# Kernel tuning notes

Hardware: AMD Instinct MI355X
Metric: run time of the kernel (lower is better)

Reference implementation:

```python
import jax, jax.numpy as jnp
import numpy as np

N = 100000
E = 1600000
F_IN, F_HID, F_OUT = 128, 64, 1


def setup_inputs() -> dict:
    key = jax.random.key(0)
    ks = jax.random.split(key, 8)
    x = jax.random.normal(ks[0], (N, F_IN), dtype=jnp.float32)
    edge_index = jax.random.randint(ks[1], (2, E), 0, N, dtype=jnp.int64)
    def glorot(k, fan_in, fan_out):
        scale = jnp.sqrt(2.0 / (fan_in + fan_out)).astype(jnp.float32)
        return jax.random.normal(k, (fan_in, fan_out), dtype=jnp.float32) * scale
    W1 = glorot(ks[2], F_IN, F_HID); b1 = jnp.zeros((F_HID,), jnp.float32)
    W2 = glorot(ks[3], F_HID, F_HID); b2 = jnp.zeros((F_HID,), jnp.float32)
    W3 = glorot(ks[4], F_HID, F_OUT); b3 = jnp.zeros((F_OUT,), jnp.float32)
    return {"x": x, "W1": W1, "b1": b1, "W2": W2, "b2": b2, "W3": W3, "b3": b3, "edge_index": edge_index}


def _gcn_norm(edge_index, n):
    # add self-loops, symmetric D^{-1/2} (A+I) D^{-1/2} normalization (PyG GCNConv default)
    loop = jnp.arange(n, dtype=edge_index.dtype)
    src = jnp.concatenate([edge_index[0], loop])
    dst = jnp.concatenate([edge_index[1], loop])
    deg = jax.ops.segment_sum(jnp.ones_like(src, dtype=jnp.float32), dst, num_segments=n)
    dis = jnp.where(deg > 0, jax.lax.rsqrt(jnp.maximum(deg, 1.0)), 0.0)
    norm = dis[src] * dis[dst]  # [E+N]
    return src, dst, norm


def _gcn_conv(h, W, b, src, dst, norm, n):
    h = h @ W                                   # [N, f_out]
    msg = h[src] * norm[:, None]                # gather + scale, [E+N, f_out]
    out = jax.ops.segment_sum(msg, dst, num_segments=n)  # scatter-add
    return out + b


def reference(x, W1, b1, W2, b2, W3, b3, edge_index):
    n = x.shape[0]
    src, dst, norm = _gcn_norm(edge_index, n)
    h = jax.nn.relu(_gcn_conv(x, W1, b1, src, dst, norm, n))
    h = jax.nn.relu(_gcn_conv(h, W2, b2, src, dst, norm, n))
    h = _gcn_conv(h, W3, b3, src, dst, norm, n)
    return jax.nn.sigmoid(h)
```

## Files before the change

kernel.cpp:

```cpp
#include <hip/hip_runtime.h>
#include <math.h>

#define NN 100000
#define NE 1600000
#define NSHARD 4
#define SHARD_W (NN / NSHARD)
#define NCHUNK 64
#define CHUNK_E (NE / NCHUNK)
#define CHUNK_I4 (CHUNK_E / 4)

typedef __attribute__((ext_vector_type(8))) short bf16x8;
typedef __attribute__((ext_vector_type(4))) float f32x4;
typedef __attribute__((ext_vector_type(2))) float f32x2;

__device__ inline unsigned f2bf(float f) {
    unsigned u = __float_as_uint(f);
    u += 0x7FFFu + ((u >> 16) & 1u);
    return u >> 16;
}
__device__ inline float bflo(unsigned v) { return __uint_as_float(v << 16); }
__device__ inline float bfhi(unsigned v) { return __uint_as_float(v & 0xFFFF0000u); }
__device__ inline f32x2 bfpair(unsigned u) {
    f32x2 r;
    r.x = __uint_as_float(u << 16);
    r.y = __uint_as_float(u & 0xFFFF0000u);
    return r;
}

__global__ __launch_bounds__(256) void k_cnt(const int4* __restrict__ dst4,
                                             unsigned char* __restrict__ cnt,
                                             unsigned char* __restrict__ lrank) {
    __shared__ __align__(16) unsigned ldeg[SHARD_W];
    int t = threadIdx.x;
    int shard = blockIdx.x & (NSHARD - 1);
    int b = blockIdx.x >> 2;
    int lo = shard * SHARD_W;
    uint4 z4 = make_uint4(0u, 0u, 0u, 0u);
    for (int i = t; i < SHARD_W / 4; i += 256) ((uint4*)ldeg)[i] = z4;
    __syncthreads();
    const int4* p = dst4 + b * CHUNK_I4;
    unsigned char* lr = lrank + b * CHUNK_E;
#pragma unroll 4
    for (int j = t; j < CHUNK_I4; j += 256) {
        int4 d = p[j];
        unsigned ex = (unsigned)(d.x - lo);
        unsigned ey = (unsigned)(d.y - lo);
        unsigned ez = (unsigned)(d.z - lo);
        unsigned ew = (unsigned)(d.w - lo);
        if (ex < SHARD_W) lr[4 * j + 0] = (unsigned char)atomicAdd(&ldeg[ex], 1u);
        if (ey < SHARD_W) lr[4 * j + 1] = (unsigned char)atomicAdd(&ldeg[ey], 1u);
        if (ez < SHARD_W) lr[4 * j + 2] = (unsigned char)atomicAdd(&ldeg[ez], 1u);
        if (ew < SHARD_W) lr[4 * j + 3] = (unsigned char)atomicAdd(&ldeg[ew], 1u);
    }
    __syncthreads();
    unsigned* cb32 = (unsigned*)cnt + b * (NN / 4) + shard * (SHARD_W / 4);
    for (int i = t; i < SHARD_W / 4; i += 256) {
        uint4 v = *(const uint4*)&ldeg[4 * i];
        cb32[i] = (v.x & 255u) | ((v.y & 255u) << 8) | ((v.z & 255u) << 16)
                | ((v.w & 255u) << 24);
    }
}

__global__ __launch_bounds__(256) void k_blkscan(unsigned char* __restrict__ cnt,
                                                 int* __restrict__ deg,
                                                 int* __restrict__ bsums) {
    __shared__ int s[256];
    int i = blockIdx.x * 256 + threadIdx.x;
    int total = 0;
    if (i < NN) {
        unsigned a = 0;
#pragma unroll
        for (int b = 0; b < NCHUNK; ++b) {
            unsigned v = cnt[b * NN + i];
            cnt[b * NN + i] = (unsigned char)a;
            a += v;
        }
        deg[i] = (int)a;
        total = (int)a;
    }
    s[threadIdx.x] = total;
    __syncthreads();
    for (int off = 128; off > 0; off >>= 1) {
        if (threadIdx.x < off) s[threadIdx.x] += s[threadIdx.x + off];
        __syncthreads();
    }
    if (threadIdx.x == 0) bsums[blockIdx.x] = s[0];
}

__global__ void k_scan512(const int* __restrict__ bsums, int* __restrict__ bscan) {
    __shared__ int s[512];
    int t = threadIdx.x;
    int v = (t < 391) ? bsums[t] : 0;
    s[t] = v;
    __syncthreads();
    for (int off = 1; off < 512; off <<= 1) {
        int x = (t >= off) ? s[t - off] : 0;
        __syncthreads();
        s[t] += x;
        __syncthreads();
    }
    bscan[t] = s[t] - v;
}

__global__ void k_rowptr(const int* __restrict__ deg, const int* __restrict__ bscan,
                         int* __restrict__ rowptr, float* __restrict__ dis) {
    __shared__ int s[256];
    int t = threadIdx.x;
    int i = blockIdx.x * 256 + t;
    int d = (i < NN) ? deg[i] : 0;
    s[t] = d;
    __syncthreads();
    for (int off = 1; off < 256; off <<= 1) {
        int x = (t >= off) ? s[t - off] : 0;
        __syncthreads();
        s[t] += x;
        __syncthreads();
    }
    if (i < NN) {
        int rp = bscan[blockIdx.x] + s[t] - d;
        rowptr[i] = rp;
        dis[i] = rsqrtf((float)(d + 1));
    }
    if (i == 0) rowptr[NN] = NE;
}

__global__ __launch_bounds__(256) void k_build_csr(
    const int4* __restrict__ src4, const int4* __restrict__ dst4,
    const unsigned char* __restrict__ blkoff, const unsigned* __restrict__ lr4,
    const int* __restrict__ rowptr, int* __restrict__ csr) {
    int shard = blockIdx.x & (NSHARD - 1);
    int bsh = blockIdx.x >> 2;
    int stride = (gridDim.x >> 2) * 256;
    int lo = shard * SHARD_W;
    const int NE4 = NE / 4;
    for (int i = bsh * 256 + threadIdx.x; i < NE4; i += stride) {
        int4 d = dst4[i];
        int4 s = src4[i];
        unsigned lr = lr4[i];
        const unsigned char* off = blkoff + (i / CHUNK_I4) * NN;
        unsigned ex = (unsigned)(d.x - lo);
        unsigned ey = (unsigned)(d.y - lo);
        unsigned ez = (unsigned)(d.z - lo);
        unsigned ew = (unsigned)(d.w - lo);
        if (ex < SHARD_W) csr[rowptr[d.x] + off[d.x] + (lr & 255u)] = s.x;
        if (ey < SHARD_W) csr[rowptr[d.y] + off[d.y] + ((lr >> 8) & 255u)] = s.y;
        if (ez < SHARD_W) csr[rowptr[d.z] + off[d.z] + ((lr >> 16) & 255u)] = s.z;
        if (ew < SHARD_W) csr[rowptr[d.w] + off[d.w] + (lr >> 24)] = s.w;
    }
}

#define XS_LD 136
__global__ __launch_bounds__(256) void k_gemm1(
    const float* __restrict__ x, const float* __restrict__ W,
    const float* __restrict__ dis, unsigned short* __restrict__ tsb) {
    __shared__ unsigned short xs[64 * XS_LD];
    __shared__ unsigned short wt[64 * XS_LD];
    int t = threadIdx.x;
    int row0 = blockIdx.x * 64;
    for (int i = t; i < 64 * 64; i += 256) {
        int n = i & 63, k2 = i >> 6;
        float w0 = W[(2 * k2) * 64 + n];
        float w1 = W[(2 * k2 + 1) * 64 + n];
        *(unsigned*)&wt[n * XS_LD + 2 * k2] = f2bf(w0) | (f2bf(w1) << 16);
    }
    for (int i = t; i < 64 * 32; i += 256) {
        int r = i >> 5, c4 = i & 31;
        int gr = row0 + r;
        uint2 p = {0u, 0u};
        if (gr < NN) {
            float4 v = *(const float4*)&x[gr * 128 + 4 * c4];
            p.x = f2bf(v.x) | (f2bf(v.y) << 16);
            p.y = f2bf(v.z) | (f2bf(v.w) << 16);
        }
        *(uint2*)&xs[r * XS_LD + 4 * c4] = p;
    }
    __syncthreads();
    int w = t >> 6, l = t & 63;
    int lm = l & 15, lg = l >> 4;
    const unsigned short* ap = &xs[(16 * w + lm) * XS_LD + 8 * lg];
    const unsigned short* bp = &wt[lm * XS_LD + 8 * lg];
    f32x4 acc0 = {0, 0, 0, 0}, acc1 = {0, 0, 0, 0}, acc2 = {0, 0, 0, 0}, acc3 = {0, 0, 0, 0};
#pragma unroll
    for (int kb = 0; kb < 4; ++kb) {
        bf16x8 a  = *(const bf16x8*)(ap + 32 * kb);
        bf16x8 b0 = *(const bf16x8*)(bp + 32 * kb);
        bf16x8 b1 = *(const bf16x8*)(bp + 16 * XS_LD + 32 * kb);
        bf16x8 b2 = *(const bf16x8*)(bp + 32 * XS_LD + 32 * kb);
        bf16x8 b3 = *(const bf16x8*)(bp + 48 * XS_LD + 32 * kb);
        acc0 = __builtin_amdgcn_mfma_f32_16x16x32_bf16(a, b0, acc0, 0, 0, 0);
        acc1 = __builtin_amdgcn_mfma_f32_16x16x32_bf16(a, b1, acc1, 0, 0, 0);
        acc2 = __builtin_amdgcn_mfma_f32_16x16x32_bf16(a, b2, acc2, 0, 0, 0);
        acc3 = __builtin_amdgcn_mfma_f32_16x16x32_bf16(a, b3, acc3, 0, 0, 0);
    }
    int rbase = row0 + 16 * w + 4 * lg;
#pragma unroll
    for (int r = 0; r < 4; ++r) {
        int row = rbase + r;
        if (row < NN) {
            float dv = dis[row];
            unsigned short* o = &tsb[row * 64 + lm];
            o[0]  = (unsigned short)f2bf(acc0[r] * dv);
            o[16] = (unsigned short)f2bf(acc1[r] * dv);
            o[32] = (unsigned short)f2bf(acc2[r] * dv);
            o[48] = (unsigned short)f2bf(acc3[r] * dv);
        }
    }
}

#define HS_LD 72
__global__ __launch_bounds__(256) void k_gemm2(
    const unsigned short* __restrict__ hb, const float* __restrict__ W,
    const float* __restrict__ dis, unsigned short* __restrict__ tsb) {
    __shared__ unsigned short hs[64 * HS_LD];
    __shared__ unsigned short wh[64 * HS_LD];
    __shared__ unsigned short wl[64 * HS_LD];
    int t = threadIdx.x;
    int row0 = blockIdx.x * 64;
    for (int i = t; i < 64 * 32; i += 256) {
        int n = i & 63, k2 = i >> 6;
        float w0 = W[(2 * k2) * 64 + n];
        float w1 = W[(2 * k2 + 1) * 64 + n];
        unsigned h0 = f2bf(w0), h1 = f2bf(w1);
        *(unsigned*)&wh[n * HS_LD + 2 * k2] = h0 | (h1 << 16);
        float r0 = w0 - bflo(h0), r1 = w1 - bflo(h1);
        *(unsigned*)&wl[n * HS_LD + 2 * k2] = f2bf(r0) | (f2bf(r1) << 16);
    }
    const uint4* h4 = (const uint4*)hb;
    for (int i = t; i < 64 * 8; i += 256) {
        int r = i >> 3, c8 = i & 7;
        int gr = row0 + r;
        uint4 v = (gr < NN) ? h4[gr * 8 + c8] : make_uint4(0u, 0u, 0u, 0u);
        *(uint4*)&hs[r * HS_LD + 8 * c8] = v;
    }
    __syncthreads();
    int w = t >> 6, l = t & 63;
    int lm = l & 15, lg = l >> 4;
    const unsigned short* ap = &hs[(16 * w + lm) * HS_LD + 8 * lg];
    const unsigned short* bh = &wh[lm * HS_LD + 8 * lg];
    const unsigned short* bl = &wl[lm * HS_LD + 8 * lg];
    f32x4 acc0 = {0, 0, 0, 0}, acc1 = {0, 0, 0, 0}, acc2 = {0, 0, 0, 0}, acc3 = {0, 0, 0, 0};
#pragma unroll
    for (int kb = 0; kb < 2; ++kb) {
        bf16x8 a  = *(const bf16x8*)(ap + 32 * kb);
        bf16x8 h0 = *(const bf16x8*)(bh + 32 * kb);
        bf16x8 h1 = *(const bf16x8*)(bh + 16 * HS_LD + 32 * kb);
        bf16x8 h2 = *(const bf16x8*)(bh + 32 * HS_LD + 32 * kb);
        bf16x8 h3 = *(const bf16x8*)(bh + 48 * HS_LD + 32 * kb);
        bf16x8 l0 = *(const bf16x8*)(bl + 32 * kb);
        bf16x8 l1 = *(const bf16x8*)(bl + 16 * HS_LD + 32 * kb);
        bf16x8 l2 = *(const bf16x8*)(bl + 32 * HS_LD + 32 * kb);
        bf16x8 l3 = *(const bf16x8*)(bl + 48 * HS_LD + 32 * kb);
        acc0 = __builtin_amdgcn_mfma_f32_16x16x32_bf16(a, h0, acc0, 0, 0, 0);
        acc1 = __builtin_amdgcn_mfma_f32_16x16x32_bf16(a, h1, acc1, 0, 0, 0);
        acc2 = __builtin_amdgcn_mfma_f32_16x16x32_bf16(a, h2, acc2, 0, 0, 0);
        acc3 = __builtin_amdgcn_mfma_f32_16x16x32_bf16(a, h3, acc3, 0, 0, 0);
        acc0 = __builtin_amdgcn_mfma_f32_16x16x32_bf16(a, l0, acc0, 0, 0, 0);
        acc1 = __builtin_amdgcn_mfma_f32_16x16x32_bf16(a, l1, acc1, 0, 0, 0);
        acc2 = __builtin_amdgcn_mfma_f32_16x16x32_bf16(a, l2, acc2, 0, 0, 0);
        acc3 = __builtin_amdgcn_mfma_f32_16x16x32_bf16(a, l3, acc3, 0, 0, 0);
    }
    int rbase = row0 + 16 * w + 4 * lg;
#pragma unroll
    for (int r = 0; r < 4; ++r) {
        int row = rbase + r;
        if (row < NN) {
            float dv = dis[row];
            unsigned short* o = &tsb[row * 64 + lm];
            o[0]  = (unsigned short)f2bf(acc0[r] * dv);
            o[16] = (unsigned short)f2bf(acc1[r] * dv);
            o[32] = (unsigned short)f2bf(acc2[r] * dv);
            o[48] = (unsigned short)f2bf(acc3[r] * dv);
        }
    }
}

#define AGG_BLOCKS 2048
__global__ __launch_bounds__(256) void k_agg_relu(
    const unsigned short* __restrict__ tsb, const int* __restrict__ rowptr,
    const int* __restrict__ csr, const float* __restrict__ dis,
    const float* __restrict__ b, unsigned short* __restrict__ hb) {
    int wid = blockIdx.x * 4 + (threadIdx.x >> 6);
    const int nwaves = AGG_BLOCKS * 4;
    int lane = threadIdx.x & 63;
    int half = lane >> 5;
    int oct = (lane >> 3) & 3;
    int fl = lane & 7;
    const uint4* ts128 = (const uint4*)tsb;
    for (int base = wid * 2; base < NN; base += nwaves * 2) {
        int node = base + half;
        bool valid = node < NN;
        f32x2 a0 = {0.f, 0.f}, a1 = {0.f, 0.f}, a2 = {0.f, 0.f}, a3 = {0.f, 0.f};
        if (valid) {
            if (oct == 0) {
                uint4 v = ts128[node * 8 + fl];
                a0 += bfpair(v.x); a1 += bfpair(v.y); a2 += bfpair(v.z); a3 += bfpair(v.w);
            }
            int e = rowptr[node] + oct, end = rowptr[node + 1];
            for (; e + 12 < end; e += 16) {
                int s0 = csr[e];
                int s1 = csr[e + 4];
                int s2 = csr[e + 8];
                int s3 = csr[e + 12];
                uint4 v0 = ts128[s0 * 8 + fl];
                uint4 v1 = ts128[s1 * 8 + fl];
                uint4 v2 = ts128[s2 * 8 + fl];
                uint4 v3 = ts128[s3 * 8 + fl];
                a0 += bfpair(v0.x); a1 += bfpair(v0.y); a2 += bfpair(v0.z); a3 += bfpair(v0.w);
                a0 += bfpair(v1.x); a1 += bfpair(v1.y); a2 += bfpair(v1.z); a3 += bfpair(v1.w);
                a0 += bfpair(v2.x); a1 += bfpair(v2.y); a2 += bfpair(v2.z); a3 += bfpair(v2.w);
                a0 += bfpair(v3.x); a1 += bfpair(v3.y); a2 += bfpair(v3.z); a3 += bfpair(v3.w);
            }
            for (; e < end; e += 4) {
                uint4 v = ts128[csr[e] * 8 + fl];
                a0 += bfpair(v.x); a1 += bfpair(v.y); a2 += bfpair(v.z); a3 += bfpair(v.w);
            }
        }
#pragma unroll
        for (int off = 8; off <= 16; off <<= 1) {
            a0.x += __shfl_xor(a0.x, off); a0.y += __shfl_xor(a0.y, off);
            a1.x += __shfl_xor(a1.x, off); a1.y += __shfl_xor(a1.y, off);
            a2.x += __shfl_xor(a2.x, off); a2.y += __shfl_xor(a2.y, off);
            a3.x += __shfl_xor(a3.x, off); a3.y += __shfl_xor(a3.y, off);
        }
        if (valid && oct == 0) {
            float dv = dis[node];
            float v0 = fmaxf(a0.x * dv + b[8 * fl + 0], 0.f);
            float v1 = fmaxf(a0.y * dv + b[8 * fl + 1], 0.f);
            float v2 = fmaxf(a1.x * dv + b[8 * fl + 2], 0.f);
            float v3 = fmaxf(a1.y * dv + b[8 * fl + 3], 0.f);
            float v4 = fmaxf(a2.x * dv + b[8 * fl + 4], 0.f);
            float v5 = fmaxf(a2.y * dv + b[8 * fl + 5], 0.f);
            float v6 = fmaxf(a3.x * dv + b[8 * fl + 6], 0.f);
            float v7 = fmaxf(a3.y * dv + b[8 * fl + 7], 0.f);
            uint4 p;
            p.x = f2bf(v0) | (f2bf(v1) << 16);
            p.y = f2bf(v2) | (f2bf(v3) << 16);
            p.z = f2bf(v4) | (f2bf(v5) << 16);
            p.w = f2bf(v6) | (f2bf(v7) << 16);
            ((uint4*)hb)[node * 8 + fl] = p;
        }
    }
}

__global__ void k_gemm3(const unsigned short* __restrict__ hb, const float* __restrict__ W3,
                        const float* __restrict__ dis, float* __restrict__ t3) {
    __shared__ float Ws[64];
    if (threadIdx.x < 64) Ws[threadIdx.x] = W3[threadIdx.x];
    __syncthreads();
    int row = blockIdx.x * 256 + threadIdx.x;
    if (row >= NN) return;
    const uint4* hp = (const uint4*)(hb + row * 64);
    float acc = 0.f;
#pragma unroll
    for (int k = 0; k < 8; ++k) {
        uint4 v = hp[k];
        acc += bflo(v.x) * Ws[8 * k + 0] + bfhi(v.x) * Ws[8 * k + 1]
             + bflo(v.y) * Ws[8 * k + 2] + bfhi(v.y) * Ws[8 * k + 3]
             + bflo(v.z) * Ws[8 * k + 4] + bfhi(v.z) * Ws[8 * k + 5]
             + bflo(v.w) * Ws[8 * k + 6] + bfhi(v.w) * Ws[8 * k + 7];
    }
    t3[row] = acc * dis[row];
}

__global__ void k_out(const float* __restrict__ t3, const int* __restrict__ rowptr,
                      const int* __restrict__ csr, const float* __restrict__ dis,
                      const float* __restrict__ b3, float* __restrict__ out) {
    int i = blockIdx.x * 256 + threadIdx.x;
    if (i >= NN) return;
    float acc = t3[i];
    float acc1 = 0.f, acc2 = 0.f, acc3 = 0.f;
    int e = rowptr[i], end = rowptr[i + 1];
    for (; e + 4 <= end; e += 4) {
        acc += t3[csr[e]];
        acc1 += t3[csr[e + 1]];
        acc2 += t3[csr[e + 2]];
        acc3 += t3[csr[e + 3]];
    }
    for (; e < end; ++e) acc += t3[csr[e]];
    float z = ((acc + acc1) + (acc2 + acc3)) * dis[i] + b3[0];
    out[i] = 1.f / (1.f + __expf(-z));
}

extern "C" void kernel_launch(void* const* d_in, const int* in_sizes, int n_in,
                              void* d_out, int out_size, void* d_ws, size_t ws_size,
                              hipStream_t stream) {
    const float* x  = (const float*)d_in[0];
    const float* W1 = (const float*)d_in[1];
    const float* b1 = (const float*)d_in[2];
    const float* W2 = (const float*)d_in[3];
    const float* b2 = (const float*)d_in[4];
    const float* W3 = (const float*)d_in[5];
    const float* b3 = (const float*)d_in[6];
    const int*   ei = (const int*)d_in[7];
    const int* src = ei;
    const int* dst = ei + NE;
    float* out = (float*)d_out;

    unsigned short* TSB = (unsigned short*)d_ws;
    unsigned short* HB  = TSB + (size_t)NN * 64;
    float* dis    = (float*)(HB + (size_t)NN * 64);
    float* t3     = dis + NN;
    int*   deg    = (int*)(t3 + NN);
    int*   rowptr = deg + NN;
    int*   bsums  = rowptr + NN + 8;
    int*   bscan  = bsums + 512;
    int*   csr    = bscan + 512;
    unsigned char* lrank = (unsigned char*)TSB;
    unsigned char* cnt   = (unsigned char*)HB;

    const int nbN = (NN + 255) / 256;
    const int nbG = (NN + 63) / 64;

    k_cnt<<<NSHARD * NCHUNK, 256, 0, stream>>>((const int4*)dst, cnt, lrank);
    k_blkscan<<<nbN, 256, 0, stream>>>(cnt, deg, bsums);
    k_scan512<<<1, 512, 0, stream>>>(bsums, bscan);
    k_rowptr<<<nbN, 256, 0, stream>>>(deg, bscan, rowptr, dis);
    k_build_csr<<<2048, 256, 0, stream>>>((const int4*)src, (const int4*)dst,
                                          cnt, (const unsigned*)lrank, rowptr, csr);

    k_gemm1<<<nbG, 256, 0, stream>>>(x, W1, dis, TSB);
    k_agg_relu<<<AGG_BLOCKS, 256, 0, stream>>>(TSB, rowptr, csr, dis, b1, HB);

    k_gemm2<<<nbG, 256, 0, stream>>>(HB, W2, dis, TSB);
    k_agg_relu<<<AGG_BLOCKS, 256, 0, stream>>>(TSB, rowptr, csr, dis, b2, HB);

    k_gemm3<<<nbN, 256, 0, stream>>>(HB, W3, dis, t3);
    k_out<<<nbN, 256, 0, stream>>>(t3, rowptr, csr, dis, b3, out);
}
```

Measured before the change: 273.2 us.

## Fuse layer-3 projection into second aggregation and fold block scan into rowptr

The second aggregate+ReLU kernel now computes the 64->1 dot product with W3 directly in registers. It reduces across lanes with shuffles and writes t3, so the separate gemm3 kernel and the bf16 HB write/read round trip go away. The single-block scan kernel is removed: each rowptr block now sums the preceding block totals itself, which adds some redundant work per block but saves a launch. The aggregation kernel also preloads bias and W3 into registers and prefetches the next node's rowptr pair. The fused path computes t3 in fp32 rather than after bf16 rounding, so numerics change slightly.

```diff
diff --git a/kernel.cpp b/kernel.cpp
--- a/kernel.cpp
+++ b/kernel.cpp
@@ -87,26 +87,22 @@
     if (threadIdx.x == 0) bsums[blockIdx.x] = s[0];
 }
 
-__global__ void k_scan512(const int* __restrict__ bsums, int* __restrict__ bscan) {
-    __shared__ int s[512];
-    int t = threadIdx.x;
-    int v = (t < 391) ? bsums[t] : 0;
-    s[t] = v;
-    __syncthreads();
-    for (int off = 1; off < 512; off <<= 1) {
-        int x = (t >= off) ? s[t - off] : 0;
-        __syncthreads();
-        s[t] += x;
-        __syncthreads();
-    }
-    bscan[t] = s[t] - v;
-}
-
-__global__ void k_rowptr(const int* __restrict__ deg, const int* __restrict__ bscan,
+__global__ void k_rowptr(const int* __restrict__ deg, const int* __restrict__ bsums,
                          int* __restrict__ rowptr, float* __restrict__ dis) {
+    __shared__ int sbase[256];
     __shared__ int s[256];
     int t = threadIdx.x;
-    int i = blockIdx.x * 256 + t;
+    int bid = blockIdx.x;
+    int v = (t < bid) ? bsums[t] : 0;
+    if (t + 256 < bid) v += bsums[t + 256];
+    sbase[t] = v;
+    __syncthreads();
+    for (int off = 128; off > 0; off >>= 1) {
+        if (t < off) sbase[t] += sbase[t + off];
+        __syncthreads();
+    }
+    int base = sbase[0];
+    int i = bid * 256 + t;
     int d = (i < NN) ? deg[i] : 0;
     s[t] = d;
     __syncthreads();
@@ -117,8 +113,7 @@
         __syncthreads();
     }
     if (i < NN) {
-        int rp = bscan[blockIdx.x] + s[t] - d;
-        rowptr[i] = rp;
+        rowptr[i] = base + s[t] - d;
         dis[i] = rsqrtf((float)(d + 1));
     }
     if (i == 0) rowptr[NN] = NE;
@@ -275,10 +270,12 @@
 }
 
 #define AGG_BLOCKS 2048
+template <bool FUSE3>
 __global__ __launch_bounds__(256) void k_agg_relu(
     const unsigned short* __restrict__ tsb, const int* __restrict__ rowptr,
     const int* __restrict__ csr, const float* __restrict__ dis,
-    const float* __restrict__ b, unsigned short* __restrict__ hb) {
+    const float* __restrict__ b, const float* __restrict__ W3,
+    unsigned short* __restrict__ hb, float* __restrict__ t3) {
     int wid = blockIdx.x * 4 + (threadIdx.x >> 6);
     const int nwaves = AGG_BLOCKS * 4;
     int lane = threadIdx.x & 63;
@@ -286,16 +283,28 @@
     int oct = (lane >> 3) & 3;
     int fl = lane & 7;
     const uint4* ts128 = (const uint4*)tsb;
+    float br[8], w3r[8];
+#pragma unroll
+    for (int j = 0; j < 8; ++j) {
+        br[j] = b[8 * fl + j];
+        if (FUSE3) w3r[j] = W3[8 * fl + j];
+    }
+    int node0 = wid * 2 + half;
+    int pr0 = 0, pr1 = 0;
+    if (node0 < NN) { pr0 = rowptr[node0]; pr1 = rowptr[node0 + 1]; }
     for (int base = wid * 2; base < NN; base += nwaves * 2) {
         int node = base + half;
         bool valid = node < NN;
+        int r0 = pr0, r1 = pr1;
+        int nnode = node + nwaves * 2;
+        if (nnode < NN) { pr0 = rowptr[nnode]; pr1 = rowptr[nnode + 1]; }
         f32x2 a0 = {0.f, 0.f}, a1 = {0.f, 0.f}, a2 = {0.f, 0.f}, a3 = {0.f, 0.f};
         if (valid) {
             if (oct == 0) {
                 uint4 v = ts128[node * 8 + fl];
                 a0 += bfpair(v.x); a1 += bfpair(v.y); a2 += bfpair(v.z); a3 += bfpair(v.w);
             }
-            int e = rowptr[node] + oct, end = rowptr[node + 1];
+            int e = r0 + oct, end = r1;
             for (; e + 12 < end; e += 16) {
                 int s0 = csr[e];
                 int s1 = csr[e + 4];
@@ -322,44 +331,33 @@
             a2.x += __shfl_xor(a2.x, off); a2.y += __shfl_xor(a2.y, off);
             a3.x += __shfl_xor(a3.x, off); a3.y += __shfl_xor(a3.y, off);
         }
-        if (valid && oct == 0) {
-            float dv = dis[node];
-            float v0 = fmaxf(a0.x * dv + b[8 * fl + 0], 0.f);
-            float v1 = fmaxf(a0.y * dv + b[8 * fl + 1], 0.f);
-            float v2 = fmaxf(a1.x * dv + b[8 * fl + 2], 0.f);
-            float v3 = fmaxf(a1.y * dv + b[8 * fl + 3], 0.f);
-            float v4 = fmaxf(a2.x * dv + b[8 * fl + 4], 0.f);
-            float v5 = fmaxf(a2.y * dv + b[8 * fl + 5], 0.f);
-            float v6 = fmaxf(a3.x * dv + b[8 * fl + 6], 0.f);
-            float v7 = fmaxf(a3.y * dv + b[8 * fl + 7], 0.f);
-            uint4 p;
-            p.x = f2bf(v0) | (f2bf(v1) << 16);
-            p.y = f2bf(v2) | (f2bf(v3) << 16);
-            p.z = f2bf(v4) | (f2bf(v5) << 16);
-            p.w = f2bf(v6) | (f2bf(v7) << 16);
-            ((uint4*)hb)[node * 8 + fl] = p;
-        }
-    }
-}
-
-__global__ void k_gemm3(const unsigned short* __restrict__ hb, const float* __restrict__ W3,
-                        const float* __restrict__ dis, float* __restrict__ t3) {
-    __shared__ float Ws[64];
-    if (threadIdx.x < 64) Ws[threadIdx.x] = W3[threadIdx.x];
-    __syncthreads();
-    int row = blockIdx.x * 256 + threadIdx.x;
-    if (row >= NN) return;
-    const uint4* hp = (const uint4*)(hb + row * 64);
-    float acc = 0.f;
-#pragma unroll
-    for (int k = 0; k < 8; ++k) {
-        uint4 v = hp[k];
-        acc += bflo(v.x) * Ws[8 * k + 0] + bfhi(v.x) * Ws[8 * k + 1]
-             + bflo(v.y) * Ws[8 * k + 2] + bfhi(v.y) * Ws[8 * k + 3]
-             + bflo(v.z) * Ws[8 * k + 4] + bfhi(v.z) * Ws[8 * k + 5]
-             + bflo(v.w) * Ws[8 * k + 6] + bfhi(v.w) * Ws[8 * k + 7];
-    }
-    t3[row] = acc * dis[row];
+        if (oct == 0) {
+            float dv = valid ? dis[node] : 0.f;
+            float v0 = fmaxf(a0.x * dv + br[0], 0.f);
+            float v1 = fmaxf(a0.y * dv + br[1], 0.f);
+            float v2 = fmaxf(a1.x * dv + br[2], 0.f);
+            float v3 = fmaxf(a1.y * dv + br[3], 0.f);
+            float v4 = fmaxf(a2.x * dv + br[4], 0.f);
+            float v5 = fmaxf(a2.y * dv + br[5], 0.f);
+            float v6 = fmaxf(a3.x * dv + br[6], 0.f);
+            float v7 = fmaxf(a3.y * dv + br[7], 0.f);
+            if (FUSE3) {
+                float part = v0 * w3r[0] + v1 * w3r[1] + v2 * w3r[2] + v3 * w3r[3]
+                           + v4 * w3r[4] + v5 * w3r[5] + v6 * w3r[6] + v7 * w3r[7];
+                part += __shfl_xor(part, 1);
+                part += __shfl_xor(part, 2);
+                part += __shfl_xor(part, 4);
+                if (valid && fl == 0) t3[node] = part * dv;
+            } else if (valid) {
+                uint4 p;
+                p.x = f2bf(v0) | (f2bf(v1) << 16);
+                p.y = f2bf(v2) | (f2bf(v3) << 16);
+                p.z = f2bf(v4) | (f2bf(v5) << 16);
+                p.w = f2bf(v6) | (f2bf(v7) << 16);
+                ((uint4*)hb)[node * 8 + fl] = p;
+            }
+        }
+    }
 }
 
 __global__ void k_out(const float* __restrict__ t3, const int* __restrict__ rowptr,
@@ -403,8 +401,7 @@
     int*   deg    = (int*)(t3 + NN);
     int*   rowptr = deg + NN;
     int*   bsums  = rowptr + NN + 8;
-    int*   bscan  = bsums + 512;
-    int*   csr    = bscan + 512;
+    int*   csr    = bsums + 512;
     unsigned char* lrank = (unsigned char*)TSB;
     unsigned char* cnt   = (unsigned char*)HB;
 
@@ -413,17 +410,15 @@
 
     k_cnt<<<NSHARD * NCHUNK, 256, 0, stream>>>((const int4*)dst, cnt, lrank);
     k_blkscan<<<nbN, 256, 0, stream>>>(cnt, deg, bsums);
-    k_scan512<<<1, 512, 0, stream>>>(bsums, bscan);
-    k_rowptr<<<nbN, 256, 0, stream>>>(deg, bscan, rowptr, dis);
+    k_rowptr<<<nbN, 256, 0, stream>>>(deg, bsums, rowptr, dis);
     k_build_csr<<<2048, 256, 0, stream>>>((const int4*)src, (const int4*)dst,
                                           cnt, (const unsigned*)lrank, rowptr, csr);
 
     k_gemm1<<<nbG, 256, 0, stream>>>(x, W1, dis, TSB);
-    k_agg_relu<<<AGG_BLOCKS, 256, 0, stream>>>(TSB, rowptr, csr, dis, b1, HB);
+    k_agg_relu<false><<<AGG_BLOCKS, 256, 0, stream>>>(TSB, rowptr, csr, dis, b1, W3, HB, t3);
 
     k_gemm2<<<nbG, 256, 0, stream>>>(HB, W2, dis, TSB);
-    k_agg_relu<<<AGG_BLOCKS, 256, 0, stream>>>(TSB, rowptr, csr, dis, b2, HB);
-
-    k_gemm3<<<nbN, 256, 0, stream>>>(HB, W3, dis, t3);
+    k_agg_relu<true><<<AGG_BLOCKS, 256, 0, stream>>>(TSB, rowptr, csr, dis, b2, W3, HB, t3);
+
     k_out<<<nbN, 256, 0, stream>>>(t3, rowptr, csr, dis, b3, out);
 }
```

Measured after the change: 280.5 us. 1.03x slower.
